# Performance work log

Measured on AMD Instinct MI355X. Metric: run time of the kernel, lower is better.

## Reference

```python
import jax, jax.numpy as jnp
import numpy as np

ALPHA = 1.0


def setup_inputs() -> dict:
    key = jax.random.key(0)
    ks = jax.random.split(key, 7)
    B, S, IN, OUT = 8, 8192, 1024, 1024
    RANK, DDIM, UDIM = 4, 100, 50
    return {
        "hidden_states": jax.random.normal(ks[0], (B, S, IN), dtype=jnp.float32),
        "W": jax.random.normal(ks[1], (OUT, IN), dtype=jnp.float32) * 0.02,
        "b": jax.random.normal(ks[2], (OUT,), dtype=jnp.float32) * 0.02,
        "lora_down": jax.random.normal(ks[3], (RANK, DDIM), dtype=jnp.float32) * 0.1,
        "lora_up": jax.random.normal(ks[4], (UDIM, RANK), dtype=jnp.float32) * 0.1,
        "down_aux": jax.random.normal(ks[5], (DDIM, IN), dtype=jnp.float32) * 0.03,
        "up_aux": jax.random.normal(ks[6], (OUT, UDIM), dtype=jnp.float32) * 0.03,
    }


def reference(hidden_states, W, b, lora_down, lora_up, down_aux, up_aux):
    # lilora_weight = up_aux @ lora_up @ lora_down @ down_aux  -> [out, in]
    lilora_weight = up_aux @ (lora_up @ (lora_down @ down_aux))
    base = jnp.einsum("bsi,oi->bso", hidden_states, W) + b
    delta = jnp.einsum("bsi,oi->bso", hidden_states, lilora_weight)
    return base + ALPHA * delta
```

## Files before the change

### kernel.cpp

```cpp
#include <hip/hip_runtime.h>
#include <hip/hip_bf16.h>
#include <stdint.h>

#define ALPHA 1.0f

typedef __attribute__((ext_vector_type(8))) short bf16x8;
typedef __attribute__((ext_vector_type(4))) float f32x4;

__device__ __forceinline__ unsigned short f32_to_bf16_rne(float f) {
    union { float f; unsigned int u; } v; v.f = f;
    unsigned int u = v.u;
    unsigned int r = u + 0x7FFFu + ((u >> 16) & 1u);
    return (unsigned short)(r >> 16);
}

__device__ __forceinline__ unsigned int cvt_pk_bf16(float lo, float hi) {
    unsigned int r;
    asm("v_cvt_pk_bf16_f32 %0, %1, %2" : "=v"(r) : "v"(lo), "v"(hi));
    return r;
}

__device__ __forceinline__ void async_copy16(const void* g, void* l) {
    __builtin_amdgcn_global_load_lds(
        (const __attribute__((address_space(1))) void*)g,
        (__attribute__((address_space(3))) void*)l, 16, 0, 0);
}

__global__ void lilora_t2_kernel(const float* __restrict__ lora_down,
                                 const float* __restrict__ lora_up,
                                 const float* __restrict__ down_aux,
                                 float* __restrict__ t2) {
    int i = threadIdx.x;
    float t1[4] = {0.f, 0.f, 0.f, 0.f};
    for (int d = 0; d < 100; ++d) {
        float da = down_aux[d * 1024 + i];
#pragma unroll
        for (int r = 0; r < 4; ++r) t1[r] += lora_down[r * 100 + d] * da;
    }
    for (int u = 0; u < 50; ++u) {
        float acc = 0.f;
#pragma unroll
        for (int r = 0; r < 4; ++r) acc += lora_up[u * 4 + r] * t1[r];
        t2[u * 1024 + i] = acc;
    }
}

__global__ __launch_bounds__(256)
void weff_bf16_kernel(const float* __restrict__ W, const float* __restrict__ up_aux,
                      const float* __restrict__ t2, unsigned short* __restrict__ weff) {
    int o = blockIdx.x;
    int i0 = threadIdx.x * 4;
    float4 acc = *(const float4*)(W + (long)o * 1024 + i0);
    for (int u = 0; u < 50; ++u) {
        float s = up_aux[o * 50 + u] * ALPHA;
        float4 t = *(const float4*)(t2 + u * 1024 + i0);
        acc.x += s * t.x; acc.y += s * t.y; acc.z += s * t.z; acc.w += s * t.w;
    }
    ushort4 r;
    r.x = f32_to_bf16_rne(acc.x);
    r.y = f32_to_bf16_rne(acc.y);
    r.z = f32_to_bf16_rne(acc.z);
    r.w = f32_to_bf16_rne(acc.w);
    *(ushort4*)(weff + (long)o * 1024 + i0) = r;
}

__global__ __launch_bounds__(256)
void weff_f32_kernel(const float* __restrict__ W, const float* __restrict__ up_aux,
                     const float* __restrict__ t2, float* __restrict__ weff) {
    int o = blockIdx.x;
    int i0 = threadIdx.x * 4;
    float4 acc = *(const float4*)(W + (long)o * 1024 + i0);
    for (int u = 0; u < 50; ++u) {
        float s = up_aux[o * 50 + u] * ALPHA;
        float4 t = *(const float4*)(t2 + u * 1024 + i0);
        acc.x += s * t.x; acc.y += s * t.y; acc.z += s * t.z; acc.w += s * t.w;
    }
    *(float4*)(weff + (long)o * 1024 + i0) = acc;
}

#define BM 128
#define BN 128
#define BK 64

__global__ __launch_bounds__(256, 2)
void gemm_fused_kernel(const float* __restrict__ A,
                       const unsigned short* __restrict__ Bt,
                       const float* __restrict__ bias,
                       float* __restrict__ C, int M, int N, int K) {
    __shared__ __align__(16) unsigned short As[2][BM * BK];
    __shared__ __align__(16) unsigned short Bs[2][BN * BK];

    int nTilesN = N / BN;
    int nwg = gridDim.x;
    int bid = blockIdx.x;
    int swz = bid;
    if ((nwg & 7) == 0) {
        int cpx = nwg >> 3;
        swz = (bid & 7) * cpx + (bid >> 3);
    }
    int tm = swz / nTilesN;
    int tn = swz % nTilesN;

    int tid = threadIdx.x;
    int lane = tid & 63;
    int wave = tid >> 6;
    int wr = wave >> 1;
    int wc = wave & 1;

    const long rowA0 = (long)tm * BM;
    const long colB0 = (long)tn * BN;

    int ar_[4], acg_[4], acl_[4];
#pragma unroll
    for (int q = 0; q < 4; ++q) {
        int p = q * 256 + tid;
        ar_[q]  = p >> 3;
        acg_[q] = p & 7;
        acl_[q] = acg_[q] ^ (ar_[q] & 7);
    }

    int brow[4], bchk[4];
#pragma unroll
    for (int q = 0; q < 4; ++q) {
        int pc = q * 256 + tid;
        brow[q] = pc >> 3;
        bchk[q] = (pc & 7) ^ (brow[q] & 7);
    }

    f32x4 acc[4][4];
#pragma unroll
    for (int m = 0; m < 4; ++m)
#pragma unroll
        for (int n = 0; n < 4; ++n) acc[m][n] = (f32x4)(0.0f);

    int fr = lane & 15;
    int h4 = lane >> 4;
    int s7 = fr & 7;

    const int nIter = K / BK;

    float4 vA0[4], vA1[4];
#pragma unroll
    for (int q = 0; q < 4; ++q) {
        const float* gp = A + (rowA0 + ar_[q]) * (long)K + acg_[q] * 8;
        vA0[q] = ((const float4*)gp)[0];
        vA1[q] = ((const float4*)gp)[1];
    }
#pragma unroll
    for (int q = 0; q < 4; ++q) {
        const unsigned short* gp = Bt + (colB0 + brow[q]) * (long)K + bchk[q] * 8;
        async_copy16(gp, (unsigned short*)Bs[0] + q * 2048 + wave * 512);
    }
#pragma unroll
    for (int q = 0; q < 4; ++q) {
        uint4 w;
        w.x = cvt_pk_bf16(vA0[q].x, vA0[q].y);
        w.y = cvt_pk_bf16(vA0[q].z, vA0[q].w);
        w.z = cvt_pk_bf16(vA1[q].x, vA1[q].y);
        w.w = cvt_pk_bf16(vA1[q].z, vA1[q].w);
        *(uint4*)(&As[0][ar_[q] * 64 + acl_[q] * 8]) = w;
    }
#pragma unroll
    for (int q = 0; q < 4; ++q) {
        const float* gp = A + (rowA0 + ar_[q]) * (long)K + BK + acg_[q] * 8;
        vA0[q] = ((const float4*)gp)[0];
        vA1[q] = ((const float4*)gp)[1];
    }
    __syncthreads();

    for (int it = 0; it < nIter; ++it) {
        int cur = it & 1;

        if (it + 1 < nIter) {
            long k1 = (long)(it + 1) * BK;
#pragma unroll
            for (int q = 0; q < 4; ++q) {
                const unsigned short* gp =
                    Bt + (colB0 + brow[q]) * (long)K + k1 + bchk[q] * 8;
                async_copy16(gp, (unsigned short*)Bs[cur ^ 1] + q * 2048 + wave * 512);
            }
        }
        if (it + 1 < nIter) {
#pragma unroll
            for (int q = 0; q < 4; ++q) {
                uint4 w;
                w.x = cvt_pk_bf16(vA0[q].x, vA0[q].y);
                w.y = cvt_pk_bf16(vA0[q].z, vA0[q].w);
                w.z = cvt_pk_bf16(vA1[q].x, vA1[q].y);
                w.w = cvt_pk_bf16(vA1[q].z, vA1[q].w);
                *(uint4*)(&As[cur ^ 1][ar_[q] * 64 + acl_[q] * 8]) = w;
            }
        }
        if (it + 2 < nIter) {
            long k2 = (long)(it + 2) * BK;
#pragma unroll
            for (int q = 0; q < 4; ++q) {
                const float* gp = A + (rowA0 + ar_[q]) * (long)K + k2 + acg_[q] * 8;
                vA0[q] = ((const float4*)gp)[0];
                vA1[q] = ((const float4*)gp)[1];
            }
        }

#pragma unroll
        for (int kk = 0; kk < 2; ++kk) {
            bf16x8 a[4], b[4];
            int cidx = kk * 4 + h4;
            int cpos = cidx ^ s7;
#pragma unroll
            for (int m = 0; m < 4; ++m) {
                int row = wr * 64 + m * 16 + fr;
                a[m] = *(const bf16x8*)(&As[cur][row * 64 + cpos * 8]);
            }
#pragma unroll
            for (int n = 0; n < 4; ++n) {
                int row = wc * 64 + n * 16 + fr;
                b[n] = *(const bf16x8*)(&Bs[cur][row * 64 + cpos * 8]);
            }
#pragma unroll
            for (int m = 0; m < 4; ++m)
#pragma unroll
                for (int n = 0; n < 4; ++n)
                    acc[m][n] = __builtin_amdgcn_mfma_f32_16x16x32_bf16(a[m], b[n], acc[m][n], 0, 0, 0);
        }

        __syncthreads();
    }

    int ccol = lane & 15;
    int crow = (lane >> 4) * 4;
#pragma unroll
    for (int m = 0; m < 4; ++m) {
        long grow = rowA0 + wr * 64 + m * 16 + crow;
#pragma unroll
        for (int n = 0; n < 4; ++n) {
            long gcol = colB0 + wc * 64 + n * 16 + ccol;
            float bb = bias[gcol];
#pragma unroll
            for (int r = 0; r < 4; ++r) {
                C[(grow + r) * N + gcol] = acc[m][n][r] + bb;
            }
        }
    }
}

__global__ __launch_bounds__(256)
void gemm_f32_fallback(const float* __restrict__ A, const float* __restrict__ Bt,
                       const float* __restrict__ bias, float* __restrict__ C,
                       int M, int N, int K) {
    __shared__ float As[64][17];
    __shared__ float Bs[64][17];
    int tilesN = N / 64;
    int tm = blockIdx.x / tilesN;
    int tn = blockIdx.x % tilesN;
    int tid = threadIdx.x;
    int tr = tid / 16, tc = tid % 16;
    float acc[4][4] = {};
    for (int k0 = 0; k0 < K; k0 += 16) {
        for (int t = tid; t < 64 * 16; t += 256) {
            int r = t / 16, c = t % 16;
            As[r][c] = A[((long)tm * 64 + r) * K + k0 + c];
            Bs[r][c] = Bt[((long)tn * 64 + r) * K + k0 + c];
        }
        __syncthreads();
#pragma unroll
        for (int kk = 0; kk < 16; ++kk) {
            float av[4], bv[4];
#pragma unroll
            for (int i = 0; i < 4; ++i) av[i] = As[tr * 4 + i][kk];
#pragma unroll
            for (int j = 0; j < 4; ++j) bv[j] = Bs[tc * 4 + j][kk];
#pragma unroll
            for (int i = 0; i < 4; ++i)
#pragma unroll
                for (int j = 0; j < 4; ++j) acc[i][j] += av[i] * bv[j];
        }
        __syncthreads();
    }
#pragma unroll
    for (int i = 0; i < 4; ++i) {
        long row = (long)tm * 64 + tr * 4 + i;
#pragma unroll
        for (int j = 0; j < 4; ++j) {
            long col = (long)tn * 64 + tc * 4 + j;
            C[row * N + col] = acc[i][j] + bias[col];
        }
    }
}

extern "C" void kernel_launch(void* const* d_in, const int* in_sizes, int n_in,
                              void* d_out, int out_size, void* d_ws, size_t ws_size,
                              hipStream_t stream) {
    const float* hs        = (const float*)d_in[0];
    const float* W         = (const float*)d_in[1];
    const float* b         = (const float*)d_in[2];
    const float* lora_down = (const float*)d_in[3];
    const float* lora_up   = (const float*)d_in[4];
    const float* down_aux  = (const float*)d_in[5];
    const float* up_aux    = (const float*)d_in[6];
    float* out = (float*)d_out;

    const int K = 1024;
    const int N = 1024;
    const int M = in_sizes[0] / K;

    char* ws = (char*)d_ws;
    float* t2 = (float*)ws;
    const size_t OFF_WEFF = 256 * 1024;
    const size_t NEED_FAST = OFF_WEFF + 2 * 1024 * 1024;

    lilora_t2_kernel<<<1, 1024, 0, stream>>>(lora_down, lora_up, down_aux, t2);

    if (ws_size >= NEED_FAST) {
        unsigned short* weff = (unsigned short*)(ws + OFF_WEFF);
        weff_bf16_kernel<<<N, 256, 0, stream>>>(W, up_aux, t2, weff);
        int grid = (M / BM) * (N / BN);
        gemm_fused_kernel<<<grid, 256, 0, stream>>>(hs, weff, b, out, M, N, K);
    } else {
        float* weff = (float*)(ws + OFF_WEFF);
        weff_f32_kernel<<<N, 256, 0, stream>>>(W, up_aux, t2, weff);
        int grid = (M / 64) * (N / 64);
        gemm_f32_fallback<<<grid, 256, 0, stream>>>(hs, weff, b, out, M, N, K);
    }
}
```

Baseline: 277.2 us.

## Single-buffer LDS tiles and raise occupancy to three workgroups per CU

Replaces the double-buffered LDS tiles for A and B with a single buffer (64KB down to 32KB per block) and raises launch bounds from 2 to 3 workgroups per CU. Each iteration now syncs, issues the async B copy and A store for the current tile, prefetches the next A tile into registers, syncs again, then runs the MFMAs. The aim is to hide latency through more resident waves instead of intra-block double buffering. The cost is that the B load is no longer overlapped with compute inside a block, and register pressure under the tighter bound may cause spills.

```diff
diff --git a/kernel.cpp b/kernel.cpp
--- a/kernel.cpp
+++ b/kernel.cpp
@@ -82,13 +82,13 @@
 #define BN 128
 #define BK 64
 
-__global__ __launch_bounds__(256, 2)
+__global__ __launch_bounds__(256, 3)
 void gemm_fused_kernel(const float* __restrict__ A,
                        const unsigned short* __restrict__ Bt,
                        const float* __restrict__ bias,
                        float* __restrict__ C, int M, int N, int K) {
-    __shared__ __align__(16) unsigned short As[2][BM * BK];
-    __shared__ __align__(16) unsigned short Bs[2][BN * BK];
+    __shared__ __align__(16) unsigned short As[BM * BK];
+    __shared__ __align__(16) unsigned short Bs[BN * BK];
 
     int nTilesN = N / BN;
     int nwg = gridDim.x;
@@ -146,75 +146,53 @@
         vA0[q] = ((const float4*)gp)[0];
         vA1[q] = ((const float4*)gp)[1];
     }
-#pragma unroll
-    for (int q = 0; q < 4; ++q) {
-        const unsigned short* gp = Bt + (colB0 + brow[q]) * (long)K + bchk[q] * 8;
-        async_copy16(gp, (unsigned short*)Bs[0] + q * 2048 + wave * 512);
-    }
-#pragma unroll
-    for (int q = 0; q < 4; ++q) {
-        uint4 w;
-        w.x = cvt_pk_bf16(vA0[q].x, vA0[q].y);
-        w.y = cvt_pk_bf16(vA0[q].z, vA0[q].w);
-        w.z = cvt_pk_bf16(vA1[q].x, vA1[q].y);
-        w.w = cvt_pk_bf16(vA1[q].z, vA1[q].w);
-        *(uint4*)(&As[0][ar_[q] * 64 + acl_[q] * 8]) = w;
-    }
-#pragma unroll
-    for (int q = 0; q < 4; ++q) {
-        const float* gp = A + (rowA0 + ar_[q]) * (long)K + BK + acg_[q] * 8;
-        vA0[q] = ((const float4*)gp)[0];
-        vA1[q] = ((const float4*)gp)[1];
-    }
-    __syncthreads();
 
     for (int it = 0; it < nIter; ++it) {
-        int cur = it & 1;
+        long k0 = (long)it * BK;
+        __syncthreads();
+
+#pragma unroll
+        for (int q = 0; q < 4; ++q) {
+            const unsigned short* gp =
+                Bt + (colB0 + brow[q]) * (long)K + k0 + bchk[q] * 8;
+            async_copy16(gp, (unsigned short*)Bs + q * 2048 + wave * 512);
+        }
+
+#pragma unroll
+        for (int q = 0; q < 4; ++q) {
+            uint4 w;
+            w.x = cvt_pk_bf16(vA0[q].x, vA0[q].y);
+            w.y = cvt_pk_bf16(vA0[q].z, vA0[q].w);
+            w.z = cvt_pk_bf16(vA1[q].x, vA1[q].y);
+            w.w = cvt_pk_bf16(vA1[q].z, vA1[q].w);
+            *(uint4*)(&As[ar_[q] * 64 + acl_[q] * 8]) = w;
+        }
 
         if (it + 1 < nIter) {
-            long k1 = (long)(it + 1) * BK;
+            long k1 = k0 + BK;
 #pragma unroll
             for (int q = 0; q < 4; ++q) {
-                const unsigned short* gp =
-                    Bt + (colB0 + brow[q]) * (long)K + k1 + bchk[q] * 8;
-                async_copy16(gp, (unsigned short*)Bs[cur ^ 1] + q * 2048 + wave * 512);
-            }
-        }
-        if (it + 1 < nIter) {
-#pragma unroll
-            for (int q = 0; q < 4; ++q) {
-                uint4 w;
-                w.x = cvt_pk_bf16(vA0[q].x, vA0[q].y);
-                w.y = cvt_pk_bf16(vA0[q].z, vA0[q].w);
-                w.z = cvt_pk_bf16(vA1[q].x, vA1[q].y);
-                w.w = cvt_pk_bf16(vA1[q].z, vA1[q].w);
-                *(uint4*)(&As[cur ^ 1][ar_[q] * 64 + acl_[q] * 8]) = w;
-            }
-        }
-        if (it + 2 < nIter) {
-            long k2 = (long)(it + 2) * BK;
-#pragma unroll
-            for (int q = 0; q < 4; ++q) {
-                const float* gp = A + (rowA0 + ar_[q]) * (long)K + k2 + acg_[q] * 8;
+                const float* gp = A + (rowA0 + ar_[q]) * (long)K + k1 + acg_[q] * 8;
                 vA0[q] = ((const float4*)gp)[0];
                 vA1[q] = ((const float4*)gp)[1];
             }
         }
 
+        __syncthreads();
+
 #pragma unroll
         for (int kk = 0; kk < 2; ++kk) {
             bf16x8 a[4], b[4];
-            int cidx = kk * 4 + h4;
-            int cpos = cidx ^ s7;
+            int cpos = (kk * 4 + h4) ^ s7;
 #pragma unroll
             for (int m = 0; m < 4; ++m) {
                 int row = wr * 64 + m * 16 + fr;
-                a[m] = *(const bf16x8*)(&As[cur][row * 64 + cpos * 8]);
+                a[m] = *(const bf16x8*)(&As[row * 64 + cpos * 8]);
             }
 #pragma unroll
             for (int n = 0; n < 4; ++n) {
                 int row = wc * 64 + n * 16 + fr;
-                b[n] = *(const bf16x8*)(&Bs[cur][row * 64 + cpos * 8]);
+                b[n] = *(const bf16x8*)(&Bs[row * 64 + cpos * 8]);
             }
 #pragma unroll
             for (int m = 0; m < 4; ++m)
@@ -222,8 +200,6 @@
                 for (int n = 0; n < 4; ++n)
                     acc[m][n] = __builtin_amdgcn_mfma_f32_16x16x32_bf16(a[m], b[n], acc[m][n], 0, 0, 0);
         }
-
-        __syncthreads();
     }
 
     int ccol = lane & 15;
```

New measurement: 273.7 us. Within noise of the previous version (-1.3%).
